# Kernel optimization log

Measured on AMD Instinct MI355X. Metric: run time of the kernel, lower is better.

## Reference

```python
import jax, jax.numpy as jnp
import numpy as np
import math

B, S, E, H = 2, 2048, 1024, 16
HD = E // H          # head_dim = 64
HX = 64              # helix_dim
P = HX // 2          # helix pairs = 32

def setup_inputs() -> dict:
    key = jax.random.key(0)
    ks = jax.random.split(key, 12)
    sc = 0.02
    return {
        "x":    jax.random.normal(ks[0], (B, S, E), dtype=jnp.float32),
        "Wq":   jax.random.normal(ks[1], (E, E), dtype=jnp.float32) * sc,
        "bq":   jnp.zeros((E,), dtype=jnp.float32),
        "Wk":   jax.random.normal(ks[2], (E, E), dtype=jnp.float32) * sc,
        "bk":   jnp.zeros((E,), dtype=jnp.float32),
        "Wv":   jax.random.normal(ks[3], (E, E), dtype=jnp.float32) * sc,
        "bv":   jnp.zeros((E,), dtype=jnp.float32),
        "Wo":   jax.random.normal(ks[4], (E, E), dtype=jnp.float32) * sc,
        "bo":   jnp.zeros((E,), dtype=jnp.float32),
        "Whel": jax.random.normal(ks[5], (H, HX, HD), dtype=jnp.float32) * sc,
        "bhel": jnp.zeros((H, HX), dtype=jnp.float32),
    }

def _l2norm(x, eps=1e-12):
    # torch F.normalize(p=2, dim=-1): x / max(||x||, eps)
    n = jnp.sqrt(jnp.sum(x * x, axis=-1, keepdims=True))
    return x / jnp.maximum(n, eps)

def _scramble(t):
    # faithful to torch: (B,S,2) -> transpose(1,2) -> reshape(B,S,2),
    # vectorized over (H,P): t is (B,H,P,S,2)
    b, h, p, s, _ = t.shape
    return jnp.swapaxes(t, -1, -2).reshape(b, h, p, s, 2)

def reference(x, Wq, bq, Wk, bk, Wv, bv, Wo, bo, Whel, bhel):
    b, s, e = x.shape
    h, hx, hd = Whel.shape
    p = hx // 2
    q = x @ Wq.T + bq
    k = x @ Wk.T + bk
    v = x @ Wv.T + bv
    qh = q.reshape(b, s, h, hd)
    kh = k.reshape(b, s, h, hd)
    # per-head helical projections: (B,S,H,HX)
    q_hel = jnp.einsum('bshd,hed->bshe', qh, Whel) + bhel
    k_hel = jnp.einsum('bshd,hed->bshe', kh, Whel) + bhel
    # split into 2D coords, normalize each pair: (B,H,P,S,2)
    qn = _l2norm(q_hel.reshape(b, s, h, p, 2)).transpose(0, 2, 3, 1, 4)
    kn = _l2norm(k_hel.reshape(b, s, h, p, 2)).transpose(0, 2, 3, 1, 4)
    qn = _scramble(qn)
    kn = _scramble(kn)
    # helical similarity averaged over pairs: (B,H,S,S)
    helical = jnp.einsum('bhpsc,bhptc->bhst', qn, kn) / p
    # standard scaled dot-product scores
    dot = jnp.einsum('bshd,bthd->bhst', qh, kh) / math.sqrt(hd)
    alpha = 0.5
    attn = jax.nn.softmax(alpha * dot + (1.0 - alpha) * helical, axis=-1)
    vh = v.reshape(b, s, h, hd)
    out = jnp.einsum('bhst,bthd->bshd', attn, vh).reshape(b, s, e)
    return out @ Wo.T + bo
```

## Files before the change

kernel.cpp:

```cpp
#include <hip/hip_runtime.h>
#include <hip/hip_bf16.h>


typedef unsigned short u16;
typedef unsigned int u32;
typedef __attribute__((ext_vector_type(8))) __bf16 bf16x8;
typedef __attribute__((ext_vector_type(4))) float f32x4;
typedef __attribute__((ext_vector_type(16))) float f32x16;

union BFrag { u32 u[4]; bf16x8 b; };

__device__ __forceinline__ u16 f2b(float f) {
  u32 u = __float_as_uint(f);
  u32 r = (u + 0x7fffu + ((u >> 16) & 1u)) >> 16;
  return (u16)r;
}
__device__ __forceinline__ float b2f(u16 h) {
  return __uint_as_float(((u32)h) << 16);
}

__device__ __forceinline__ f32x4 mfma16(bf16x8 a, bf16x8 b, f32x4 c) {
  return __builtin_amdgcn_mfma_f32_16x16x32_bf16(a, b, c, 0, 0, 0);
}
__device__ __forceinline__ f32x16 mfma32(bf16x8 a, bf16x8 b, f32x16 c) {
  return __builtin_amdgcn_mfma_f32_32x32x16_bf16(a, b, c, 0, 0, 0);
}

__device__ __forceinline__ void gld16(void* lds, const void* g) {
  __builtin_amdgcn_global_load_lds(
      (const __attribute__((address_space(1))) unsigned int*)g,
      (__attribute__((address_space(3))) unsigned int*)lds, 16, 0, 0);
}

#define LOG2E 1.4426950408889634f

__global__ __launch_bounds__(256) void cast_kernel(
    const float* __restrict__ x,  const float* __restrict__ wq,
    const float* __restrict__ wk, const float* __restrict__ wv,
    const float* __restrict__ wo, const float* __restrict__ whel,
    u16* __restrict__ xb, u16* __restrict__ wb, u16* __restrict__ wob,
    u16* __restrict__ whb) {
  long long q = (long long)blockIdx.x * 256 + threadIdx.x;
  const float* s; u16* d; long long base;
  if (q < 1048576)      { s = x;    d = xb;            base = 0; }
  else if (q < 1310720) { s = wq;   d = wb;            base = 1048576; }
  else if (q < 1572864) { s = wk;   d = wb + 1048576;  base = 1310720; }
  else if (q < 1835008) { s = wv;   d = wb + 2097152;  base = 1572864; }
  else if (q < 2097152) { s = wo;   d = wob;           base = 1835008; }
  else                  { s = whel; d = whb;           base = 2097152; }
  long long e = (q - base) * 4;
  float4 v = *(const float4*)(s + e);
  ushort4 o;
  o.x = f2b(v.x); o.y = f2b(v.y); o.z = f2b(v.z); o.w = f2b(v.w);
  *(ushort4*)(d + e) = o;
}

__global__ __launch_bounds__(256, 3) void qkv_gemm(
    const u16* __restrict__ xb, const u16* __restrict__ wb,
    const float* __restrict__ bq, const float* __restrict__ bk,
    const float* __restrict__ bv,
    u16* __restrict__ Qcat, u16* __restrict__ Kcat, u16* __restrict__ vt) {
  __shared__ u16 Al[2][128][32];
  __shared__ u16 Bl[2][128][32];
  __shared__ u16 T[64][136];
  const int nt = blockIdx.x, mt = blockIdx.y;
  const int which = nt >> 3;
  const int n0 = (nt & 7) << 7;
  const int m0 = mt << 7;
  const int tid = threadIdx.x;
  const int wave = tid >> 6, lane = tid & 63;
  const int g = lane >> 4, c15 = lane & 15;
  const int wm = wave & 1, wn = wave >> 1;
  const u16* Wp = wb + (long long)which * (1024 * 1024) + n0 * 1024;
  const u16* Ap = xb + m0 * 1024;
  const int srow = (wave * 64 + lane) >> 2;
  const int scol = (lane & 3) << 3;

  f32x4 acc[4][4];
#pragma unroll
  for (int i = 0; i < 4; i++)
#pragma unroll
    for (int j = 0; j < 4; j++) acc[i][j] = f32x4{0.f, 0.f, 0.f, 0.f};

  gld16(&Al[0][srow][scol],      Ap + srow * 1024 + scol);
  gld16(&Al[0][64 + srow][scol], Ap + (64 + srow) * 1024 + scol);
  gld16(&Bl[0][srow][scol],      Wp + srow * 1024 + scol);
  gld16(&Bl[0][64 + srow][scol], Wp + (64 + srow) * 1024 + scol);

  for (int k0 = 0; k0 < 1024; k0 += 32) {
    const int c = (k0 >> 5) & 1;
    __syncthreads();
    if (k0 + 32 < 1024) {
      const int kn = k0 + 32;
      gld16(&Al[c ^ 1][srow][scol],      Ap + srow * 1024 + kn + scol);
      gld16(&Al[c ^ 1][64 + srow][scol], Ap + (64 + srow) * 1024 + kn + scol);
      gld16(&Bl[c ^ 1][srow][scol],      Wp + srow * 1024 + kn + scol);
      gld16(&Bl[c ^ 1][64 + srow][scol], Wp + (64 + srow) * 1024 + kn + scol);
    }
    bf16x8 a[4], b[4];
#pragma unroll
    for (int i = 0; i < 4; i++)
      a[i] = *(const bf16x8*)&Al[c][wm * 64 + i * 16 + c15][g * 8];
#pragma unroll
    for (int j = 0; j < 4; j++)
      b[j] = *(const bf16x8*)&Bl[c][wn * 64 + j * 16 + c15][g * 8];
#pragma unroll
    for (int i = 0; i < 4; i++)
#pragma unroll
      for (int j = 0; j < 4; j++) acc[i][j] = mfma16(a[i], b[j], acc[i][j]);
  }

  if (which == 2) {
#pragma unroll
    for (int half = 0; half < 2; ++half) {
      __syncthreads();
      if (wn == half) {
#pragma unroll
        for (int i = 0; i < 4; i++)
#pragma unroll
          for (int j = 0; j < 4; j++)
#pragma unroll
            for (int r = 0; r < 4; r++) {
              int nloc = j * 16 + c15;
              int mloc = wm * 64 + i * 16 + g * 4 + r;
              float v = acc[i][j][r] + bv[n0 + half * 64 + nloc];
              T[nloc][mloc] = f2b(v);
            }
      }
      __syncthreads();
#pragma unroll
      for (int it = 0; it < 4; ++it) {
        int idx = it * 256 + tid;
        int row = idx >> 4;
        int cm = (idx & 15) * 8;
        int col = n0 + half * 64 + row;
        int hh = col >> 6, dd = col & 63;
        int m = m0 + cm;
        int bb2 = m >> 11, s = m & 2047;
        *(uint4*)&vt[(((bb2 * 16 + hh) * 64) + dd) * 2048 + s] =
            *(const uint4*)&T[row][cm];
      }
    }
    return;
  }

  const float* bias = (which == 0) ? bq : bk;
#pragma unroll
  for (int i = 0; i < 4; i++)
#pragma unroll
    for (int j = 0; j < 4; j++)
#pragma unroll
      for (int r = 0; r < 4; r++) {
        int row = m0 + wm * 64 + i * 16 + g * 4 + r;
        int col = n0 + wn * 64 + j * 16 + c15;
        float v = acc[i][j][r] + bias[col];
        int bb = row >> 11, s = row & 2047;
        int hh = col >> 6, d = col & 63;
        if (which == 0) {
          Qcat[(((bb * 16 + hh) * 2048) + s) * 128 + d] =
              f2b(v * (0.0625f * LOG2E));
        } else {
          Kcat[(((bb * 16 + hh) * 2048) + s) * 128 + d] = f2b(v);
        }
      }
}

__global__ __launch_bounds__(256, 2) void helical_kernel(
    u16* __restrict__ Qcat, u16* __restrict__ Kcat,
    const u16* __restrict__ whb, const float* __restrict__ bhel) {
  __shared__ u16 A[2][2][64][32];
  __shared__ u16 Wl[2][64][32];
  const int sb = blockIdx.x, bh = blockIdx.y;
  const int h = bh & 15;
  const int s0 = sb << 6;
  const int tid = threadIdx.x;
  const int wave = tid >> 6, lane = tid & 63;
  const int g = lane >> 4, c15 = lane & 15;
  u16* Qb = Qcat + (long long)bh * (2048 * 128);
  u16* Kb = Kcat + (long long)bh * (2048 * 128);

#pragma unroll
  for (int it = 0; it < 2; ++it) {
    int cidx = it * 256 + tid;
    int e = cidx >> 3, ds = (cidx & 7) << 3;
    uint4 vv = *(const uint4*)(whb + h * 4096 + e * 64 + ds);
    *(uint4*)&Wl[ds >> 5][e][ds & 31] = vv;
  }
#pragma unroll
  for (int it = 0; it < 4; ++it) {
    int cidx = it * 256 + tid;
    int which = cidx >> 9;
    int r = (cidx >> 3) & 63;
    int ds = (cidx & 7) << 3;
    const u16* src = (which ? Kb : Qb) + (s0 + r) * 128 + ds;
    uint4 vv = *(const uint4*)src;
    if (which == 0) {
      u16 tmp[8];
      *(uint4*)tmp = vv;
#pragma unroll
      for (int q = 0; q < 8; ++q)
        tmp[q] = f2b(b2f(tmp[q]) * (16.0f / LOG2E));
      vv = *(uint4*)tmp;
    }
    *(uint4*)&A[which][ds >> 5][r][ds & 31] = vv;
  }
  __syncthreads();

  const int which = wave >> 1, hf = wave & 1;
  f32x4 acc[2][4];
#pragma unroll
  for (int i = 0; i < 2; i++)
#pragma unroll
    for (int j = 0; j < 4; j++) acc[i][j] = f32x4{0.f, 0.f, 0.f, 0.f};
#pragma unroll
  for (int kq = 0; kq < 2; ++kq) {
    bf16x8 a0 = *(const bf16x8*)&A[which][kq][hf * 32 + c15][g * 8];
    bf16x8 a1 = *(const bf16x8*)&A[which][kq][hf * 32 + 16 + c15][g * 8];
#pragma unroll
    for (int j = 0; j < 4; ++j) {
      bf16x8 bb = *(const bf16x8*)&Wl[kq][j * 16 + c15][g * 8];
      acc[0][j] = mfma16(a0, bb, acc[0][j]);
      acc[1][j] = mfma16(a1, bb, acc[1][j]);
    }
  }
  u16* Dst = which ? Kb : Qb;
  const float oscale = which ? 0.125f : (0.125f * LOG2E);
#pragma unroll
  for (int i = 0; i < 2; ++i)
#pragma unroll
    for (int j = 0; j < 4; ++j)
#pragma unroll
      for (int r = 0; r < 4; ++r) {
        int s_loc = hf * 32 + i * 16 + g * 4 + r;
        int e = j * 16 + c15;
        float v = acc[i][j][r] + bhel[h * 64 + e];
        float pp = __shfl_xor(v, 1);
        float nn = sqrtf(v * v + pp * pp);
        float o = v / fmaxf(nn, 1e-12f) * oscale;
        int s = s0 + s_loc;
        int u = s >> 1, c2 = s & 1;
        int row_out = ((e & 1) ? 1024 : 0) + u;
        int col_out = 64 + (e & ~1) + c2;
        Dst[row_out * 128 + col_out] = f2b(o);
      }
}

__global__ __launch_bounds__(512, 4) void attn_kernel(
    const u16* __restrict__ Qcat, const u16* __restrict__ Kcat,
    const u16* __restrict__ vt, u16* __restrict__ AO) {
  __shared__ u16 Kl[2][64][128];
  __shared__ u16 Vl[2][64][64];
  __shared__ float denl[2][128];
  const int qt = blockIdx.x, bh = blockIdx.y;
  const int bb = bh >> 4, h = bh & 15;
  const int q0 = qt << 7;
  const int tid = threadIdx.x;
  const int w = tid >> 6, lane = tid & 63;
  const int wq = w & 3, wt = w >> 2;
  const int l31 = lane & 31, l5 = lane >> 5;
  const u16* Qb = Qcat + (long long)bh * (2048 * 128);
  const u16* Kb = Kcat + (long long)bh * (2048 * 128);
  const u16* Vb = vt + (long long)bh * (64 * 2048);

  bf16x8 qf[8];
  {
    const u16* qrow = Qb + (q0 + 32 * wq + l31) * 128 + l5 * 8;
#pragma unroll
    for (int ks = 0; ks < 8; ++ks) qf[ks] = *(const bf16x8*)(qrow + ks * 16);
  }

  const int ll = tid;
  const int krow0 = ll >> 4;
  const int kp = ll & 15;
  const int ksrc0 = (kp & 8) | ((kp & 7) ^ (krow0 & 7));
  const int krow1 = 32 + krow0;
  const int ksrc1 = (kp & 8) | ((kp & 7) ^ (krow1 & 7));
  const int vd = ll >> 3;
  const int vsrc = (ll & 7) ^ (vd & 7);

  gld16(((u16*)Kl[0]) + ll * 8,        Kb + krow0 * 128 + ksrc0 * 8);
  gld16(((u16*)Kl[0]) + 4096 + ll * 8, Kb + krow1 * 128 + ksrc1 * 8);
  gld16(((u16*)Vl[0]) + ll * 8,        Vb + vd * 2048 + vsrc * 8);

  f32x16 accO0, accO1;
#pragma unroll
  for (int i = 0; i < 16; ++i) { accO0[i] = 0.f; accO1[i] = 0.f; }
  float den = 0.f;

  const int krow = 32 * wt + l31;
  const int kr7 = krow & 7;

  for (int t = 0; t < 32; ++t) {
    const int cur = t & 1;
    __syncthreads();
    if (t + 1 < 32) {
      const int t1 = (t + 1) << 6;
      u16* Kd = (u16*)Kl[cur ^ 1];
      gld16(Kd + ll * 8,        Kb + (t1 + krow0) * 128 + ksrc0 * 8);
      gld16(Kd + 4096 + ll * 8, Kb + (t1 + krow1) * 128 + ksrc1 * 8);
      gld16(((u16*)Vl[cur ^ 1]) + ll * 8, Vb + vd * 2048 + t1 + vsrc * 8);
    }

    f32x16 accS;
#pragma unroll
    for (int i = 0; i < 16; ++i) accS[i] = 0.f;
#pragma unroll
    for (int ks = 0; ks < 8; ++ks) {
      int lc = 2 * ks + l5;
      int p = (lc & 8) | ((lc & 7) ^ kr7);
      bf16x8 ak = *(const bf16x8*)&Kl[cur][krow][p * 8];
      accS = mfma32(ak, qf[ks], accS);
    }

    u32 D0[2], D1[2], D2[2], D3[2];
#pragma unroll
    for (int rr = 0; rr < 4; ++rr) {
      float p0 = __builtin_amdgcn_exp2f(accS[4 * rr + 0]);
      float p1 = __builtin_amdgcn_exp2f(accS[4 * rr + 1]);
      float p2 = __builtin_amdgcn_exp2f(accS[4 * rr + 2]);
      float p3 = __builtin_amdgcn_exp2f(accS[4 * rr + 3]);
      den += (p0 + p1) + (p2 + p3);
      u32 lo = (__float_as_uint(p0) >> 16) | (__float_as_uint(p1) & 0xffff0000u);
      u32 hi = (__float_as_uint(p2) >> 16) | (__float_as_uint(p3) & 0xffff0000u);
      if (rr == 0) { D0[0] = lo; D0[1] = hi; }
      else if (rr == 1) { D1[0] = lo; D1[1] = hi; }
      else if (rr == 2) { D2[0] = lo; D2[1] = hi; }
      else { D3[0] = lo; D3[1] = hi; }
    }
    BFrag A0, A1;
    {
      u32 e00 = __shfl_xor((int)D0[0], 32), e01 = __shfl_xor((int)D0[1], 32);
      u32 e10 = __shfl_xor((int)D1[0], 32), e11 = __shfl_xor((int)D1[1], 32);
      u32 e20 = __shfl_xor((int)D2[0], 32), e21 = __shfl_xor((int)D2[1], 32);
      u32 e30 = __shfl_xor((int)D3[0], 32), e31 = __shfl_xor((int)D3[1], 32);
      A0.u[0] = l5 ? e10 : D0[0];
      A0.u[1] = l5 ? e11 : D0[1];
      A0.u[2] = l5 ? D1[0] : e00;
      A0.u[3] = l5 ? D1[1] : e01;
      A1.u[0] = l5 ? e30 : D2[0];
      A1.u[1] = l5 ? e31 : D2[1];
      A1.u[2] = l5 ? D3[0] : e20;
      A1.u[3] = l5 ? D3[1] : e21;
    }

#pragma unroll
    for (int dq = 0; dq < 2; ++dq) {
      int d = 32 * dq + l31;
      int d7 = d & 7;
#pragma unroll
      for (int ks = 0; ks < 2; ++ks) {
        int lc = 4 * wt + 2 * ks + l5;
        bf16x8 bvf = *(const bf16x8*)&Vl[cur][d][((lc ^ d7) & 7) * 8];
        if (dq == 0) accO0 = mfma32(ks ? A1.b : A0.b, bvf, accO0);
        else         accO1 = mfma32(ks ? A1.b : A0.b, bvf, accO1);
      }
    }
  }

  den += __shfl_xor(den, 32);
  if (lane < 32) denl[wt][32 * wq + lane] = den;
  __syncthreads();

  float* S = (float*)Kl;
  if (wt == 1) {
#pragma unroll
    for (int r = 0; r < 16; ++r) {
      int qr = (r & 3) + 8 * (r >> 2) + 4 * l5;
      S[(wq * 32 + qr) * 64 + l31] = accO0[r];
      S[(wq * 32 + qr) * 64 + 32 + l31] = accO1[r];
    }
  }
  __syncthreads();
  if (wt == 0) {
#pragma unroll
    for (int r = 0; r < 16; ++r) {
      int qr = (r & 3) + 8 * (r >> 2) + 4 * l5;
      int ql = 32 * wq + qr;
      float inv = 1.0f / (denl[0][ql] + denl[1][ql]);
      float o0 = (accO0[r] + S[(wq * 32 + qr) * 64 + l31]) * inv;
      float o1 = (accO1[r] + S[(wq * 32 + qr) * 64 + 32 + l31]) * inv;
      long long base = ((long long)(bb * 2048 + q0 + ql) * 1024) + h * 64;
      AO[base + l31] = f2b(o0);
      AO[base + 32 + l31] = f2b(o1);
    }
  }
}

__global__ __launch_bounds__(256, 2) void out_gemm(
    const u16* __restrict__ AO, const u16* __restrict__ wob,
    const float* __restrict__ bo, float* __restrict__ out) {
  __shared__ u16 Al[2][128][32];
  __shared__ u16 Bl[2][128][32];
  const int n0 = blockIdx.x << 7;
  const int m0 = blockIdx.y << 7;
  const int tid = threadIdx.x;
  const int wave = tid >> 6, lane = tid & 63;
  const int g = lane >> 4, c15 = lane & 15;
  const int wm = wave & 1, wn = wave >> 1;
  const u16* Wp = wob + n0 * 1024;
  const u16* Ap = AO + m0 * 1024;
  const int srow = (wave * 64 + lane) >> 2;
  const int scol = (lane & 3) << 3;

  f32x4 acc[4][4];
#pragma unroll
  for (int i = 0; i < 4; i++)
#pragma unroll
    for (int j = 0; j < 4; j++) acc[i][j] = f32x4{0.f, 0.f, 0.f, 0.f};

  gld16(&Al[0][srow][scol],      Ap + srow * 1024 + scol);
  gld16(&Al[0][64 + srow][scol], Ap + (64 + srow) * 1024 + scol);
  gld16(&Bl[0][srow][scol],      Wp + srow * 1024 + scol);
  gld16(&Bl[0][64 + srow][scol], Wp + (64 + srow) * 1024 + scol);

  for (int k0 = 0; k0 < 1024; k0 += 32) {
    const int c = (k0 >> 5) & 1;
    __syncthreads();
    if (k0 + 32 < 1024) {
      const int kn = k0 + 32;
      gld16(&Al[c ^ 1][srow][scol],      Ap + srow * 1024 + kn + scol);
      gld16(&Al[c ^ 1][64 + srow][scol], Ap + (64 + srow) * 1024 + kn + scol);
      gld16(&Bl[c ^ 1][srow][scol],      Wp + srow * 1024 + kn + scol);
      gld16(&Bl[c ^ 1][64 + srow][scol], Wp + (64 + srow) * 1024 + kn + scol);
    }
    bf16x8 a[4], b[4];
#pragma unroll
    for (int i = 0; i < 4; i++)
      a[i] = *(const bf16x8*)&Al[c][wm * 64 + i * 16 + c15][g * 8];
#pragma unroll
    for (int j = 0; j < 4; j++)
      b[j] = *(const bf16x8*)&Bl[c][wn * 64 + j * 16 + c15][g * 8];
#pragma unroll
    for (int i = 0; i < 4; i++)
#pragma unroll
      for (int j = 0; j < 4; j++) acc[i][j] = mfma16(a[i], b[j], acc[i][j]);
  }
#pragma unroll
  for (int i = 0; i < 4; i++)
#pragma unroll
    for (int j = 0; j < 4; j++)
#pragma unroll
      for (int r = 0; r < 4; r++) {
        int row = m0 + wm * 64 + i * 16 + g * 4 + r;
        int col = n0 + wn * 64 + j * 16 + c15;
        out[row * 1024 + col] = acc[i][j][r] + bo[col];
      }
}

extern "C" void kernel_launch(void* const* d_in, const int* in_sizes, int n_in,
                              void* d_out, int out_size, void* d_ws,
                              size_t ws_size, hipStream_t stream) {
  const float* x    = (const float*)d_in[0];
  const float* Wq   = (const float*)d_in[1];
  const float* bq   = (const float*)d_in[2];
  const float* Wk   = (const float*)d_in[3];
  const float* bk   = (const float*)d_in[4];
  const float* Wv   = (const float*)d_in[5];
  const float* bv   = (const float*)d_in[6];
  const float* Wo   = (const float*)d_in[7];
  const float* bo   = (const float*)d_in[8];
  const float* Whel = (const float*)d_in[9];
  const float* bhel = (const float*)d_in[10];
  float* out = (float*)d_out;

  char* ws = (char*)d_ws;
  u16* xb   = (u16*)(ws + 0);
  u16* wb   = (u16*)(ws + 8388608);
  u16* wob  = (u16*)(ws + 14680064);
  u16* whb  = (u16*)(ws + 16777216);
  u16* Qcat = (u16*)(ws + 16908288);
  u16* Kcat = (u16*)(ws + 33685504);
  u16* vt   = (u16*)(ws + 50462720);
  u16* AO   = (u16*)(ws + 58851328);

  cast_kernel<<<dim3(8256), dim3(256), 0, stream>>>(x, Wq, Wk, Wv, Wo, Whel,
                                                    xb, wb, wob, whb);
  qkv_gemm<<<dim3(24, 32), dim3(256), 0, stream>>>(xb, wb, bq, bk, bv, Qcat,
                                                   Kcat, vt);
  helical_kernel<<<dim3(32, 32), dim3(256), 0, stream>>>(Qcat, Kcat, whb,
                                                         bhel);
  attn_kernel<<<dim3(16, 32), dim3(512), 0, stream>>>(Qcat, Kcat, vt, AO);
  out_gemm<<<dim3(8, 32), dim3(256), 0, stream>>>(AO, wob, bo, out);
}
```

Baseline: 226.4 us.

## Halve attention block threads and give each wave two query tiles

Reorganizes the attention kernel so each of 4 waves processes 64 query rows as two 32-row tiles, reusing each K fragment for two MFMAs and each V fragment for two outputs. This halves shared-memory reads per MFMA and spreads the K/V tile loads over fewer threads with more loads each. In exchange, per-wave register use roughly doubles for accumulators and Q fragments, and resident waves per CU drop, reducing latency hiding.

```diff
diff --git a/kernel.cpp b/kernel.cpp
--- a/kernel.cpp
+++ b/kernel.cpp
@@ -245,7 +245,7 @@
       }
 }
 
-__global__ __launch_bounds__(512, 4) void attn_kernel(
+__global__ __launch_bounds__(256, 2) void attn_kernel(
     const u16* __restrict__ Qcat, const u16* __restrict__ Kcat,
     const u16* __restrict__ vt, u16* __restrict__ AO) {
   __shared__ u16 Kl[2][64][128];
@@ -256,36 +256,55 @@
   const int q0 = qt << 7;
   const int tid = threadIdx.x;
   const int w = tid >> 6, lane = tid & 63;
-  const int wq = w & 3, wt = w >> 2;
+  const int wq2 = w & 1, wt = w >> 1;
   const int l31 = lane & 31, l5 = lane >> 5;
   const u16* Qb = Qcat + (long long)bh * (2048 * 128);
   const u16* Kb = Kcat + (long long)bh * (2048 * 128);
   const u16* Vb = vt + (long long)bh * (64 * 2048);
 
-  bf16x8 qf[8];
-  {
-    const u16* qrow = Qb + (q0 + 32 * wq + l31) * 128 + l5 * 8;
-#pragma unroll
-    for (int ks = 0; ks < 8; ++ks) qf[ks] = *(const bf16x8*)(qrow + ks * 16);
-  }
-
-  const int ll = tid;
-  const int krow0 = ll >> 4;
-  const int kp = ll & 15;
-  const int ksrc0 = (kp & 8) | ((kp & 7) ^ (krow0 & 7));
-  const int krow1 = 32 + krow0;
-  const int ksrc1 = (kp & 8) | ((kp & 7) ^ (krow1 & 7));
-  const int vd = ll >> 3;
-  const int vsrc = (ll & 7) ^ (vd & 7);
-
-  gld16(((u16*)Kl[0]) + ll * 8,        Kb + krow0 * 128 + ksrc0 * 8);
-  gld16(((u16*)Kl[0]) + 4096 + ll * 8, Kb + krow1 * 128 + ksrc1 * 8);
-  gld16(((u16*)Vl[0]) + ll * 8,        Vb + vd * 2048 + vsrc * 8);
-
-  f32x16 accO0, accO1;
-#pragma unroll
-  for (int i = 0; i < 16; ++i) { accO0[i] = 0.f; accO1[i] = 0.f; }
-  float den = 0.f;
+  bf16x8 qf[2][8];
+#pragma unroll
+  for (int qh = 0; qh < 2; ++qh) {
+    const u16* qrow = Qb + (q0 + 64 * wq2 + 32 * qh + l31) * 128 + l5 * 8;
+#pragma unroll
+    for (int ks = 0; ks < 8; ++ks)
+      qf[qh][ks] = *(const bf16x8*)(qrow + ks * 16);
+  }
+
+  int krowR[4], ksrcR[4];
+#pragma unroll
+  for (int rk = 0; rk < 4; ++rk) {
+    int id = rk * 256 + tid;
+    int row = id >> 4, kp = id & 15;
+    krowR[rk] = row;
+    ksrcR[rk] = (kp & 8) | ((kp & 7) ^ (row & 7));
+  }
+  int vdR[2], vsrcR[2];
+#pragma unroll
+  for (int rv = 0; rv < 2; ++rv) {
+    int id = rv * 256 + tid;
+    int d = id >> 3;
+    vdR[rv] = d;
+    vsrcR[rv] = (id & 7) ^ (d & 7);
+  }
+
+#pragma unroll
+  for (int rk = 0; rk < 4; ++rk)
+    gld16(((u16*)Kl[0]) + (rk * 256 + tid) * 8,
+          Kb + krowR[rk] * 128 + ksrcR[rk] * 8);
+#pragma unroll
+  for (int rv = 0; rv < 2; ++rv)
+    gld16(((u16*)Vl[0]) + (rv * 256 + tid) * 8,
+          Vb + vdR[rv] * 2048 + vsrcR[rv] * 8);
+
+  f32x16 accO[2][2];
+#pragma unroll
+  for (int a = 0; a < 2; ++a)
+#pragma unroll
+    for (int b = 0; b < 2; ++b)
+#pragma unroll
+      for (int i = 0; i < 16; ++i) accO[a][b][i] = 0.f;
+  float den[2] = {0.f, 0.f};
 
   const int krow = 32 * wt + l31;
   const int kr7 = krow & 7;
@@ -296,51 +315,62 @@
     if (t + 1 < 32) {
       const int t1 = (t + 1) << 6;
       u16* Kd = (u16*)Kl[cur ^ 1];
-      gld16(Kd + ll * 8,        Kb + (t1 + krow0) * 128 + ksrc0 * 8);
-      gld16(Kd + 4096 + ll * 8, Kb + (t1 + krow1) * 128 + ksrc1 * 8);
-      gld16(((u16*)Vl[cur ^ 1]) + ll * 8, Vb + vd * 2048 + t1 + vsrc * 8);
-    }
-
-    f32x16 accS;
-#pragma unroll
-    for (int i = 0; i < 16; ++i) accS[i] = 0.f;
+      u16* Vd = (u16*)Vl[cur ^ 1];
+#pragma unroll
+      for (int rk = 0; rk < 4; ++rk)
+        gld16(Kd + (rk * 256 + tid) * 8,
+              Kb + (t1 + krowR[rk]) * 128 + ksrcR[rk] * 8);
+#pragma unroll
+      for (int rv = 0; rv < 2; ++rv)
+        gld16(Vd + (rv * 256 + tid) * 8,
+              Vb + vdR[rv] * 2048 + t1 + vsrcR[rv] * 8);
+    }
+
+    f32x16 accS0, accS1;
+#pragma unroll
+    for (int i = 0; i < 16; ++i) { accS0[i] = 0.f; accS1[i] = 0.f; }
 #pragma unroll
     for (int ks = 0; ks < 8; ++ks) {
       int lc = 2 * ks + l5;
       int p = (lc & 8) | ((lc & 7) ^ kr7);
       bf16x8 ak = *(const bf16x8*)&Kl[cur][krow][p * 8];
-      accS = mfma32(ak, qf[ks], accS);
-    }
-
-    u32 D0[2], D1[2], D2[2], D3[2];
-#pragma unroll
-    for (int rr = 0; rr < 4; ++rr) {
-      float p0 = __builtin_amdgcn_exp2f(accS[4 * rr + 0]);
-      float p1 = __builtin_amdgcn_exp2f(accS[4 * rr + 1]);
-      float p2 = __builtin_amdgcn_exp2f(accS[4 * rr + 2]);
-      float p3 = __builtin_amdgcn_exp2f(accS[4 * rr + 3]);
-      den += (p0 + p1) + (p2 + p3);
-      u32 lo = (__float_as_uint(p0) >> 16) | (__float_as_uint(p1) & 0xffff0000u);
-      u32 hi = (__float_as_uint(p2) >> 16) | (__float_as_uint(p3) & 0xffff0000u);
-      if (rr == 0) { D0[0] = lo; D0[1] = hi; }
-      else if (rr == 1) { D1[0] = lo; D1[1] = hi; }
-      else if (rr == 2) { D2[0] = lo; D2[1] = hi; }
-      else { D3[0] = lo; D3[1] = hi; }
-    }
-    BFrag A0, A1;
-    {
+      accS0 = mfma32(ak, qf[0][ks], accS0);
+      accS1 = mfma32(ak, qf[1][ks], accS1);
+    }
+
+    BFrag PA[2][2];
+#pragma unroll
+    for (int qh = 0; qh < 2; ++qh) {
+      const f32x16& s = qh ? accS1 : accS0;
+      u32 D0[2], D1[2], D2[2], D3[2];
+#pragma unroll
+      for (int rr = 0; rr < 4; ++rr) {
+        float p0 = __builtin_amdgcn_exp2f(s[4 * rr + 0]);
+        float p1 = __builtin_amdgcn_exp2f(s[4 * rr + 1]);
+        float p2 = __builtin_amdgcn_exp2f(s[4 * rr + 2]);
+        float p3 = __builtin_amdgcn_exp2f(s[4 * rr + 3]);
+        den[qh] += (p0 + p1) + (p2 + p3);
+        u32 lo =
+            (__float_as_uint(p0) >> 16) | (__float_as_uint(p1) & 0xffff0000u);
+        u32 hi =
+            (__float_as_uint(p2) >> 16) | (__float_as_uint(p3) & 0xffff0000u);
+        if (rr == 0) { D0[0] = lo; D0[1] = hi; }
+        else if (rr == 1) { D1[0] = lo; D1[1] = hi; }
+        else if (rr == 2) { D2[0] = lo; D2[1] = hi; }
+        else { D3[0] = lo; D3[1] = hi; }
+      }
       u32 e00 = __shfl_xor((int)D0[0], 32), e01 = __shfl_xor((int)D0[1], 32);
       u32 e10 = __shfl_xor((int)D1[0], 32), e11 = __shfl_xor((int)D1[1], 32);
       u32 e20 = __shfl_xor((int)D2[0], 32), e21 = __shfl_xor((int)D2[1], 32);
       u32 e30 = __shfl_xor((int)D3[0], 32), e31 = __shfl_xor((int)D3[1], 32);
-      A0.u[0] = l5 ? e10 : D0[0];
-      A0.u[1] = l5 ? e11 : D0[1];
-      A0.u[2] = l5 ? D1[0] : e00;
-      A0.u[3] = l5 ? D1[1] : e01;
-      A1.u[0] = l5 ? e30 : D2[0];
-      A1.u[1] = l5 ? e31 : D2[1];
-      A1.u[2] = l5 ? D3[0] : e20;
-      A1.u[3] = l5 ? D3[1] : e21;
+      PA[qh][0].u[0] = l5 ? e10 : D0[0];
+      PA[qh][0].u[1] = l5 ? e11 : D0[1];
+      PA[qh][0].u[2] = l5 ? D1[0] : e00;
+      PA[qh][0].u[3] = l5 ? D1[1] : e01;
+      PA[qh][1].u[0] = l5 ? e30 : D2[0];
+      PA[qh][1].u[1] = l5 ? e31 : D2[1];
+      PA[qh][1].u[2] = l5 ? D3[0] : e20;
+      PA[qh][1].u[3] = l5 ? D3[1] : e21;
     }
 
 #pragma unroll
@@ -351,38 +381,48 @@
       for (int ks = 0; ks < 2; ++ks) {
         int lc = 4 * wt + 2 * ks + l5;
         bf16x8 bvf = *(const bf16x8*)&Vl[cur][d][((lc ^ d7) & 7) * 8];
-        if (dq == 0) accO0 = mfma32(ks ? A1.b : A0.b, bvf, accO0);
-        else         accO1 = mfma32(ks ? A1.b : A0.b, bvf, accO1);
-      }
-    }
-  }
-
-  den += __shfl_xor(den, 32);
-  if (lane < 32) denl[wt][32 * wq + lane] = den;
+        accO[0][dq] = mfma32(PA[0][ks].b, bvf, accO[0][dq]);
+        accO[1][dq] = mfma32(PA[1][ks].b, bvf, accO[1][dq]);
+      }
+    }
+  }
+
+  den[0] += __shfl_xor(den[0], 32);
+  den[1] += __shfl_xor(den[1], 32);
+  if (l5 == 0) {
+    denl[wt][64 * wq2 + l31] = den[0];
+    denl[wt][64 * wq2 + 32 + l31] = den[1];
+  }
   __syncthreads();
 
   float* S = (float*)Kl;
   if (wt == 1) {
 #pragma unroll
-    for (int r = 0; r < 16; ++r) {
-      int qr = (r & 3) + 8 * (r >> 2) + 4 * l5;
-      S[(wq * 32 + qr) * 64 + l31] = accO0[r];
-      S[(wq * 32 + qr) * 64 + 32 + l31] = accO1[r];
-    }
+    for (int qh = 0; qh < 2; ++qh)
+#pragma unroll
+      for (int dq = 0; dq < 2; ++dq)
+#pragma unroll
+        for (int r = 0; r < 16; ++r) {
+          int qr = (r & 3) + 8 * (r >> 2) + 4 * l5;
+          S[(64 * wq2 + 32 * qh + qr) * 64 + 32 * dq + l31] = accO[qh][dq][r];
+        }
   }
   __syncthreads();
   if (wt == 0) {
 #pragma unroll
-    for (int r = 0; r < 16; ++r) {
-      int qr = (r & 3) + 8 * (r >> 2) + 4 * l5;
-      int ql = 32 * wq + qr;
-      float inv = 1.0f / (denl[0][ql] + denl[1][ql]);
-      float o0 = (accO0[r] + S[(wq * 32 + qr) * 64 + l31]) * inv;
-      float o1 = (accO1[r] + S[(wq * 32 + qr) * 64 + 32 + l31]) * inv;
-      long long base = ((long long)(bb * 2048 + q0 + ql) * 1024) + h * 64;
-      AO[base + l31] = f2b(o0);
-      AO[base + 32 + l31] = f2b(o1);
-    }
+    for (int qh = 0; qh < 2; ++qh)
+#pragma unroll
+      for (int r = 0; r < 16; ++r) {
+        int qr = (r & 3) + 8 * (r >> 2) + 4 * l5;
+        int ql = 64 * wq2 + 32 * qh + qr;
+        float inv = 1.0f / (denl[0][ql] + denl[1][ql]);
+        long long base = ((long long)(bb * 2048 + q0 + ql) * 1024) + h * 64;
+#pragma unroll
+        for (int dq = 0; dq < 2; ++dq) {
+          float o = (accO[qh][dq][r] + S[ql * 64 + 32 * dq + l31]) * inv;
+          AO[base + 32 * dq + l31] = f2b(o);
+        }
+      }
   }
 }
 
@@ -479,6 +519,6 @@
                                                    Kcat, vt);
   helical_kernel<<<dim3(32, 32), dim3(256), 0, stream>>>(Qcat, Kcat, whb,
                                                          bhel);
-  attn_kernel<<<dim3(16, 32), dim3(512), 0, stream>>>(Qcat, Kcat, vt, AO);
+  attn_kernel<<<dim3(16, 32), dim3(256), 0, stream>>>(Qcat, Kcat, vt, AO);
   out_gemm<<<dim3(8, 32), dim3(256), 0, stream>>>(AO, wob, bo, out);
 }
```

Result: slower. 232.1 us (+2.5%).

## Fuse helical projection into QKV GEMM epilogue and halve out_gemm N tile

Applied to the files above, without the earlier changes.

Removes the separate helical kernel. The Q/K tiles of the QKV GEMM now compute the per-head helical projection, pair normalization and scrambled store directly from the accumulators, using shared memory that reuses the GEMM buffers via a union. This avoids re-reading Q/K from global memory and one kernel launch, but it lengthens the epilogue and adds LDS traffic in the QKV kernel. Separately, the output GEMM tile narrows from 128 to 64 columns, doubling the grid to 512 blocks for better CU occupancy at the cost of more A-tile reloads.

```diff
diff --git a/kernel.cpp b/kernel.cpp
--- a/kernel.cpp
+++ b/kernel.cpp
@@ -58,11 +58,14 @@
 __global__ __launch_bounds__(256, 3) void qkv_gemm(
     const u16* __restrict__ xb, const u16* __restrict__ wb,
     const float* __restrict__ bq, const float* __restrict__ bk,
-    const float* __restrict__ bv,
+    const float* __restrict__ bv, const u16* __restrict__ whb,
+    const float* __restrict__ bhel,
     u16* __restrict__ Qcat, u16* __restrict__ Kcat, u16* __restrict__ vt) {
-  __shared__ u16 Al[2][128][32];
-  __shared__ u16 Bl[2][128][32];
-  __shared__ u16 T[64][136];
+  union SM {
+    struct { u16 Al[2][128][32]; u16 Bl[2][128][32]; u16 T[64][136]; } m;
+    struct { u16 Th[4][32][80]; u16 Whl[2][64][80]; } e;
+  };
+  __shared__ SM sm;
   const int nt = blockIdx.x, mt = blockIdx.y;
   const int which = nt >> 3;
   const int n0 = (nt & 7) << 7;
@@ -82,28 +85,30 @@
 #pragma unroll
     for (int j = 0; j < 4; j++) acc[i][j] = f32x4{0.f, 0.f, 0.f, 0.f};
 
-  gld16(&Al[0][srow][scol],      Ap + srow * 1024 + scol);
-  gld16(&Al[0][64 + srow][scol], Ap + (64 + srow) * 1024 + scol);
-  gld16(&Bl[0][srow][scol],      Wp + srow * 1024 + scol);
-  gld16(&Bl[0][64 + srow][scol], Wp + (64 + srow) * 1024 + scol);
+  gld16(&sm.m.Al[0][srow][scol],      Ap + srow * 1024 + scol);
+  gld16(&sm.m.Al[0][64 + srow][scol], Ap + (64 + srow) * 1024 + scol);
+  gld16(&sm.m.Bl[0][srow][scol],      Wp + srow * 1024 + scol);
+  gld16(&sm.m.Bl[0][64 + srow][scol], Wp + (64 + srow) * 1024 + scol);
 
   for (int k0 = 0; k0 < 1024; k0 += 32) {
     const int c = (k0 >> 5) & 1;
     __syncthreads();
     if (k0 + 32 < 1024) {
       const int kn = k0 + 32;
-      gld16(&Al[c ^ 1][srow][scol],      Ap + srow * 1024 + kn + scol);
-      gld16(&Al[c ^ 1][64 + srow][scol], Ap + (64 + srow) * 1024 + kn + scol);
-      gld16(&Bl[c ^ 1][srow][scol],      Wp + srow * 1024 + kn + scol);
-      gld16(&Bl[c ^ 1][64 + srow][scol], Wp + (64 + srow) * 1024 + kn + scol);
+      gld16(&sm.m.Al[c ^ 1][srow][scol],      Ap + srow * 1024 + kn + scol);
+      gld16(&sm.m.Al[c ^ 1][64 + srow][scol],
+            Ap + (64 + srow) * 1024 + kn + scol);
+      gld16(&sm.m.Bl[c ^ 1][srow][scol],      Wp + srow * 1024 + kn + scol);
+      gld16(&sm.m.Bl[c ^ 1][64 + srow][scol],
+            Wp + (64 + srow) * 1024 + kn + scol);
     }
     bf16x8 a[4], b[4];
 #pragma unroll
     for (int i = 0; i < 4; i++)
-      a[i] = *(const bf16x8*)&Al[c][wm * 64 + i * 16 + c15][g * 8];
+      a[i] = *(const bf16x8*)&sm.m.Al[c][wm * 64 + i * 16 + c15][g * 8];
 #pragma unroll
     for (int j = 0; j < 4; j++)
-      b[j] = *(const bf16x8*)&Bl[c][wn * 64 + j * 16 + c15][g * 8];
+      b[j] = *(const bf16x8*)&sm.m.Bl[c][wn * 64 + j * 16 + c15][g * 8];
 #pragma unroll
     for (int i = 0; i < 4; i++)
 #pragma unroll
@@ -124,7 +129,7 @@
               int nloc = j * 16 + c15;
               int mloc = wm * 64 + i * 16 + g * 4 + r;
               float v = acc[i][j][r] + bv[n0 + half * 64 + nloc];
-              T[nloc][mloc] = f2b(v);
+              sm.m.T[nloc][mloc] = f2b(v);
             }
       }
       __syncthreads();
@@ -138,111 +143,86 @@
         int m = m0 + cm;
         int bb2 = m >> 11, s = m & 2047;
         *(uint4*)&vt[(((bb2 * 16 + hh) * 64) + dd) * 2048 + s] =
-            *(const uint4*)&T[row][cm];
+            *(const uint4*)&sm.m.T[row][cm];
       }
     }
     return;
   }
 
   const float* bias = (which == 0) ? bq : bk;
-#pragma unroll
-  for (int i = 0; i < 4; i++)
-#pragma unroll
-    for (int j = 0; j < 4; j++)
-#pragma unroll
-      for (int r = 0; r < 4; r++) {
-        int row = m0 + wm * 64 + i * 16 + g * 4 + r;
-        int col = n0 + wn * 64 + j * 16 + c15;
-        float v = acc[i][j][r] + bias[col];
-        int bb = row >> 11, s = row & 2047;
-        int hh = col >> 6, d = col & 63;
-        if (which == 0) {
-          Qcat[(((bb * 16 + hh) * 2048) + s) * 128 + d] =
-              f2b(v * (0.0625f * LOG2E));
-        } else {
-          Kcat[(((bb * 16 + hh) * 2048) + s) * 128 + d] = f2b(v);
+  const float fold = (which == 0) ? (0.0625f * LOG2E) : 1.0f;
+  const float osc  = (which == 0) ? (0.125f * LOG2E) : 0.125f;
+  const int hsel = (n0 >> 6) + wn;
+  u16* Dst = ((which == 0) ? Qcat : Kcat);
+
+  __syncthreads();
+#pragma unroll
+  for (int it = 0; it < 4; ++it) {
+    int idx = it * 256 + tid;
+    int hh = idx >> 9;
+    int e = (idx >> 3) & 63;
+    int ck = idx & 7;
+    int hg = (n0 >> 6) + hh;
+    *(uint4*)&sm.e.Whl[hh][e][ck * 8] =
+        *(const uint4*)(whb + hg * 4096 + e * 64 + ck * 8);
+  }
+  __syncthreads();
+
+#pragma unroll
+  for (int half = 0; half < 2; ++half) {
+#pragma unroll
+    for (int i2 = 0; i2 < 2; ++i2) {
+      int i = half * 2 + i2;
+#pragma unroll
+      for (int j = 0; j < 4; ++j)
+#pragma unroll
+        for (int r = 0; r < 4; ++r) {
+          int row = m0 + wm * 64 + i * 16 + g * 4 + r;
+          int col = n0 + wn * 64 + j * 16 + c15;
+          float vraw = acc[i][j][r] + bias[col];
+          int bb = row >> 11, s = row & 2047;
+          int d = col & 63;
+          Dst[(((long long)(bb * 16 + hsel) * 2048) + s) * 128 + d] =
+              f2b(vraw * fold);
+          sm.e.Th[wave][i2 * 16 + g * 4 + r][j * 16 + c15] = f2b(vraw);
         }
+    }
+    f32x4 hacc[2][4];
+#pragma unroll
+    for (int mf = 0; mf < 2; ++mf)
+#pragma unroll
+      for (int nf = 0; nf < 4; ++nf) hacc[mf][nf] = f32x4{0.f, 0.f, 0.f, 0.f};
+#pragma unroll
+    for (int kh = 0; kh < 2; ++kh) {
+      bf16x8 a0 = *(const bf16x8*)&sm.e.Th[wave][c15][kh * 32 + g * 8];
+      bf16x8 a1 = *(const bf16x8*)&sm.e.Th[wave][16 + c15][kh * 32 + g * 8];
+#pragma unroll
+      for (int nf = 0; nf < 4; ++nf) {
+        bf16x8 bwh =
+            *(const bf16x8*)&sm.e.Whl[wn][nf * 16 + c15][kh * 32 + g * 8];
+        hacc[0][nf] = mfma16(a0, bwh, hacc[0][nf]);
+        hacc[1][nf] = mfma16(a1, bwh, hacc[1][nf]);
       }
-}
-
-__global__ __launch_bounds__(256, 2) void helical_kernel(
-    u16* __restrict__ Qcat, u16* __restrict__ Kcat,
-    const u16* __restrict__ whb, const float* __restrict__ bhel) {
-  __shared__ u16 A[2][2][64][32];
-  __shared__ u16 Wl[2][64][32];
-  const int sb = blockIdx.x, bh = blockIdx.y;
-  const int h = bh & 15;
-  const int s0 = sb << 6;
-  const int tid = threadIdx.x;
-  const int wave = tid >> 6, lane = tid & 63;
-  const int g = lane >> 4, c15 = lane & 15;
-  u16* Qb = Qcat + (long long)bh * (2048 * 128);
-  u16* Kb = Kcat + (long long)bh * (2048 * 128);
-
-#pragma unroll
-  for (int it = 0; it < 2; ++it) {
-    int cidx = it * 256 + tid;
-    int e = cidx >> 3, ds = (cidx & 7) << 3;
-    uint4 vv = *(const uint4*)(whb + h * 4096 + e * 64 + ds);
-    *(uint4*)&Wl[ds >> 5][e][ds & 31] = vv;
-  }
-#pragma unroll
-  for (int it = 0; it < 4; ++it) {
-    int cidx = it * 256 + tid;
-    int which = cidx >> 9;
-    int r = (cidx >> 3) & 63;
-    int ds = (cidx & 7) << 3;
-    const u16* src = (which ? Kb : Qb) + (s0 + r) * 128 + ds;
-    uint4 vv = *(const uint4*)src;
-    if (which == 0) {
-      u16 tmp[8];
-      *(uint4*)tmp = vv;
-#pragma unroll
-      for (int q = 0; q < 8; ++q)
-        tmp[q] = f2b(b2f(tmp[q]) * (16.0f / LOG2E));
-      vv = *(uint4*)tmp;
-    }
-    *(uint4*)&A[which][ds >> 5][r][ds & 31] = vv;
-  }
-  __syncthreads();
-
-  const int which = wave >> 1, hf = wave & 1;
-  f32x4 acc[2][4];
-#pragma unroll
-  for (int i = 0; i < 2; i++)
-#pragma unroll
-    for (int j = 0; j < 4; j++) acc[i][j] = f32x4{0.f, 0.f, 0.f, 0.f};
-#pragma unroll
-  for (int kq = 0; kq < 2; ++kq) {
-    bf16x8 a0 = *(const bf16x8*)&A[which][kq][hf * 32 + c15][g * 8];
-    bf16x8 a1 = *(const bf16x8*)&A[which][kq][hf * 32 + 16 + c15][g * 8];
-#pragma unroll
-    for (int j = 0; j < 4; ++j) {
-      bf16x8 bb = *(const bf16x8*)&Wl[kq][j * 16 + c15][g * 8];
-      acc[0][j] = mfma16(a0, bb, acc[0][j]);
-      acc[1][j] = mfma16(a1, bb, acc[1][j]);
-    }
-  }
-  u16* Dst = which ? Kb : Qb;
-  const float oscale = which ? 0.125f : (0.125f * LOG2E);
-#pragma unroll
-  for (int i = 0; i < 2; ++i)
-#pragma unroll
-    for (int j = 0; j < 4; ++j)
-#pragma unroll
-      for (int r = 0; r < 4; ++r) {
-        int s_loc = hf * 32 + i * 16 + g * 4 + r;
-        int e = j * 16 + c15;
-        float v = acc[i][j][r] + bhel[h * 64 + e];
-        float pp = __shfl_xor(v, 1);
-        float nn = sqrtf(v * v + pp * pp);
-        float o = v / fmaxf(nn, 1e-12f) * oscale;
-        int s = s0 + s_loc;
-        int u = s >> 1, c2 = s & 1;
-        int row_out = ((e & 1) ? 1024 : 0) + u;
-        int col_out = 64 + (e & ~1) + c2;
-        Dst[row_out * 128 + col_out] = f2b(o);
-      }
+    }
+#pragma unroll
+    for (int mf = 0; mf < 2; ++mf)
+#pragma unroll
+      for (int nf = 0; nf < 4; ++nf)
+#pragma unroll
+        for (int r = 0; r < 4; ++r) {
+          int e = nf * 16 + c15;
+          float v = hacc[mf][nf][r] + bhel[hsel * 64 + e];
+          float pp = __shfl_xor(v, 1);
+          float nn = sqrtf(v * v + pp * pp);
+          float o = v / fmaxf(nn, 1e-12f) * osc;
+          int tok = m0 + wm * 64 + half * 32 + mf * 16 + g * 4 + r;
+          int bb = tok >> 11, s = tok & 2047;
+          int row_out = ((e & 1) ? 1024 : 0) + (s >> 1);
+          int col_out = 64 + (e & ~1) + (s & 1);
+          Dst[(((long long)(bb * 16 + hsel) * 2048) + row_out) * 128 +
+              col_out] = f2b(o);
+        }
+  }
 }
 
 __global__ __launch_bounds__(512, 4) void attn_kernel(
@@ -390,8 +370,8 @@
     const u16* __restrict__ AO, const u16* __restrict__ wob,
     const float* __restrict__ bo, float* __restrict__ out) {
   __shared__ u16 Al[2][128][32];
-  __shared__ u16 Bl[2][128][32];
-  const int n0 = blockIdx.x << 7;
+  __shared__ u16 Bl[2][64][32];
+  const int n0 = blockIdx.x << 6;
   const int m0 = blockIdx.y << 7;
   const int tid = threadIdx.x;
   const int wave = tid >> 6, lane = tid & 63;
@@ -399,19 +379,18 @@
   const int wm = wave & 1, wn = wave >> 1;
   const u16* Wp = wob + n0 * 1024;
   const u16* Ap = AO + m0 * 1024;
-  const int srow = (wave * 64 + lane) >> 2;
-  const int scol = (lane & 3) << 3;
-
-  f32x4 acc[4][4];
+  const int srow = tid >> 2;
+  const int scol = (tid & 3) << 3;
+
+  f32x4 acc[4][2];
 #pragma unroll
   for (int i = 0; i < 4; i++)
 #pragma unroll
-    for (int j = 0; j < 4; j++) acc[i][j] = f32x4{0.f, 0.f, 0.f, 0.f};
+    for (int j = 0; j < 2; j++) acc[i][j] = f32x4{0.f, 0.f, 0.f, 0.f};
 
   gld16(&Al[0][srow][scol],      Ap + srow * 1024 + scol);
   gld16(&Al[0][64 + srow][scol], Ap + (64 + srow) * 1024 + scol);
   gld16(&Bl[0][srow][scol],      Wp + srow * 1024 + scol);
-  gld16(&Bl[0][64 + srow][scol], Wp + (64 + srow) * 1024 + scol);
 
   for (int k0 = 0; k0 < 1024; k0 += 32) {
     const int c = (k0 >> 5) & 1;
@@ -421,28 +400,27 @@
       gld16(&Al[c ^ 1][srow][scol],      Ap + srow * 1024 + kn + scol);
       gld16(&Al[c ^ 1][64 + srow][scol], Ap + (64 + srow) * 1024 + kn + scol);
       gld16(&Bl[c ^ 1][srow][scol],      Wp + srow * 1024 + kn + scol);
-      gld16(&Bl[c ^ 1][64 + srow][scol], Wp + (64 + srow) * 1024 + kn + scol);
-    }
-    bf16x8 a[4], b[4];
+    }
+    bf16x8 a[4], b[2];
 #pragma unroll
     for (int i = 0; i < 4; i++)
       a[i] = *(const bf16x8*)&Al[c][wm * 64 + i * 16 + c15][g * 8];
 #pragma unroll
-    for (int j = 0; j < 4; j++)
-      b[j] = *(const bf16x8*)&Bl[c][wn * 64 + j * 16 + c15][g * 8];
+    for (int j = 0; j < 2; j++)
+      b[j] = *(const bf16x8*)&Bl[c][wn * 32 + j * 16 + c15][g * 8];
 #pragma unroll
     for (int i = 0; i < 4; i++)
 #pragma unroll
-      for (int j = 0; j < 4; j++) acc[i][j] = mfma16(a[i], b[j], acc[i][j]);
+      for (int j = 0; j < 2; j++) acc[i][j] = mfma16(a[i], b[j], acc[i][j]);
   }
 #pragma unroll
   for (int i = 0; i < 4; i++)
 #pragma unroll
-    for (int j = 0; j < 4; j++)
+    for (int j = 0; j < 2; j++)
 #pragma unroll
       for (int r = 0; r < 4; r++) {
         int row = m0 + wm * 64 + i * 16 + g * 4 + r;
-        int col = n0 + wn * 64 + j * 16 + c15;
+        int col = n0 + wn * 32 + j * 16 + c15;
         out[row * 1024 + col] = acc[i][j][r] + bo[col];
       }
 }
@@ -475,10 +453,8 @@
 
   cast_kernel<<<dim3(8256), dim3(256), 0, stream>>>(x, Wq, Wk, Wv, Wo, Whel,
                                                     xb, wb, wob, whb);
-  qkv_gemm<<<dim3(24, 32), dim3(256), 0, stream>>>(xb, wb, bq, bk, bv, Qcat,
-                                                   Kcat, vt);
-  helical_kernel<<<dim3(32, 32), dim3(256), 0, stream>>>(Qcat, Kcat, whb,
-                                                         bhel);
+  qkv_gemm<<<dim3(24, 32), dim3(256), 0, stream>>>(xb, wb, bq, bk, bv, whb,
+                                                   bhel, Qcat, Kcat, vt);
   attn_kernel<<<dim3(16, 32), dim3(512), 0, stream>>>(Qcat, Kcat, vt, AO);
-  out_gemm<<<dim3(8, 32), dim3(256), 0, stream>>>(AO, wob, bo, out);
-}
+  out_gemm<<<dim3(16, 32), dim3(256), 0, stream>>>(AO, wob, bo, out);
+}
```

Measured after the change: 227.5 us. About the same (+0.5%).
